# Optimization experiments

Measured on AMD Instinct MI355X. Metric: run time of the kernel, lower is better.

## Reference

```python
import jax, jax.numpy as jnp
import numpy as np

BETA = 0.25  # commitment_beta


def setup_inputs() -> dict:
    key = jax.random.key(0)
    k1, k2 = jax.random.split(key)
    x = jax.random.normal(k1, (16, 256, 32, 32), dtype=jnp.float32)
    # codebook weight: (n_embed + 1, embed_dim); last row is the padding idx (zeros)
    weight = jax.random.normal(k2, (8193, 256), dtype=jnp.float32) * 0.05
    weight = weight.at[-1].set(0.0)
    return {"x": x, "weight": weight}


def reference(x, weight):
    # Eval-mode forward of VectorQuantize2 (accept_image_fmap=True, no EMA update).
    B, C, H, W = x.shape
    xf = jnp.transpose(x, (0, 2, 3, 1)).reshape(B, H * W, C)  # b (h w) c
    emb = weight[:-1]  # [N, C], drop padding row
    # squared euclidean distance; argmin identical to torch.cdist argmin
    d2 = (
        jnp.sum(xf * xf, axis=-1, keepdims=True)
        - 2.0 * jnp.einsum("bnc,kc->bnk", xf, emb)
        + jnp.sum(emb * emb, axis=-1)
    )  # [B, HW, N]
    code = jnp.argmin(d2, axis=-1)  # [B, HW]
    x_q = emb[code]  # [B, HW, C]
    loss = BETA * jnp.mean((jax.lax.stop_gradient(x_q) - xf) ** 2) + jnp.mean(
        (x_q - jax.lax.stop_gradient(xf)) ** 2
    )
    # straight-through estimator
    xq_st = xf + jax.lax.stop_gradient(x_q - xf)
    xq_out = jnp.transpose(xq_st.reshape(B, H, W, C), (0, 3, 1, 2))  # b c h w
    code_out = code.reshape(B, H, W)
    return xq_out, loss, code_out
```

## Files before the change

kernel.cpp:

```cpp
#include <hip/hip_runtime.h>
#include <hip/hip_bf16.h>


#define N_ROWS   16384
#define KCODES   8192
#define DIM      256
#define LOSS_OFF 4194304
#define CODE_OFF 4194305
#define MARGIN_ACC 0.006f

typedef _Float16 half8  __attribute__((ext_vector_type(8)));
typedef _Float16 half4v __attribute__((ext_vector_type(4)));
typedef float    float4v __attribute__((ext_vector_type(4)));
typedef unsigned long long u64;

__device__ __forceinline__ unsigned umax32(unsigned a, unsigned b) { return a > b ? a : b; }
__device__ __forceinline__ unsigned umin32(unsigned a, unsigned b) { return a < b ? a : b; }
__device__ __forceinline__ void gll16(const _Float16* g, _Float16* l) {
  __builtin_amdgcn_global_load_lds((const __attribute__((address_space(1))) void*)g,
                                   (__attribute__((address_space(3))) void*)l, 16, 0, 0);
}


__global__ __launch_bounds__(256) void k_prep(const float* __restrict__ x, _Float16* __restrict__ xh,
                                              const float* __restrict__ wt, _Float16* __restrict__ eh,
                                              float* __restrict__ en2c, double* __restrict__ dacc) {
  __shared__ float lsx[128 * 65];
  __shared__ __align__(16) _Float16 ls[8192];
  __shared__ float es[32];
  int t = threadIdx.x;
  int lane = t & 63, wv = t >> 6;
  if (blockIdx.x < 128) {
    int blk  = blockIdx.x;
    int row0 = blk * 128;
    int b    = row0 >> 10;
    int n0   = row0 & 1023;
    const float* xb = x + (size_t)b * 262144 + n0;
    int n_l = t & 127, cg = t >> 7;
    float sxx = 0.f;
    for (int cc = 0; cc < 4; ++cc) {
      if (cc) __syncthreads();
      for (int j = 0; j < 32; ++j) {
        int c = cc * 64 + cg * 32 + j;
        float v = xb[(size_t)c * 1024 + n_l];
        sxx = fmaf(v, v, sxx);
        lsx[n_l * 65 + (c & 63)] = v;
      }
      __syncthreads();
#pragma unroll
      for (int i = 0; i < 4; ++i) {
        int unit = i * 256 + t;
        int rl = unit >> 3, p = unit & 7;
        const float* src = &lsx[rl * 65 + p * 8];
        half8 h;
#pragma unroll
        for (int k2 = 0; k2 < 8; ++k2) h[k2] = (_Float16)src[k2];
        int p7 = p ^ (rl & 7);
        *(half8*)&xh[(size_t)blk * 32768 + (size_t)cc * 8192 + (size_t)rl * 64 + p7 * 8] = h;
      }
    }
#pragma unroll
    for (int d = 32; d; d >>= 1) sxx += __shfl_xor(sxx, d);
    __syncthreads();
    if (lane == 0) lsx[wv] = sxx;
    __syncthreads();
    if (t == 0) atomicAdd(&dacc[0], (double)(lsx[0] + lsx[1] + lsx[2] + lsx[3]));
  } else {
    int blk  = blockIdx.x - 128;
    int k0 = blk * 32;
    const float* wb = wt + (size_t)k0 * 256;
    for (int i = 0; i < 8; ++i) {
      int lin = i * 1024 + t * 4;
      float4v v = *(const float4v*)&wb[lin];
      half4v h; float ss = 0.f;
#pragma unroll
      for (int j = 0; j < 4; ++j) { h[j] = (_Float16)v[j]; ss = fmaf(v[j], v[j], ss); }
      *(half4v*)&ls[lin] = h;
#pragma unroll
      for (int d = 32; d; d >>= 1) ss += __shfl_xor(ss, d);
      if (lane == 0) es[i * 4 + wv] = ss;
    }
    __syncthreads();
    size_t tb = (size_t)(k0 >> 7) * 32768;
    for (int i = 0; i < 4; ++i) {
      int u = i * 256 + t;
      int code_l = u >> 5;
      int cu = u & 31, chunk = cu >> 3, p = cu & 7;
      int kgl = k0 + code_l;
      int kg = p ^ (kgl & 7);
      half8 h = *(half8*)&ls[code_l * 256 + chunk * 64 + kg * 8];
      *(half8*)&eh[tb + (size_t)chunk * 8192 + (size_t)(kgl & 127) * 64 + p * 8] = h;
    }
    if (t < 32) en2c[k0 + t] = 32.0f - 0.5f * es[t];
  }
}

__global__ __launch_bounds__(256) void k_gemm(const _Float16* __restrict__ xh, const _Float16* __restrict__ eh,
                                              const float* __restrict__ en2c,
                                              u64* __restrict__ top2) {
  __shared__ __align__(16) _Float16 As[8192];
  __shared__ __align__(16) _Float16 Bs[8192];
  int t    = threadIdx.x;
  int bx   = blockIdx.x;
  int by   = blockIdx.y;
  int lane = t & 63, w = t >> 6;
  int wr = w & 1, wc = w >> 1;
  int ln15 = lane & 15, q = lane >> 4;
  int q4 = q * 4;

  const _Float16* Ag = eh + (size_t)bx * 32768;
  const _Float16* Bg = xh + (size_t)by * 32768;

  int kwave = bx * 128 + wr * 64;
  float4v cin[4];
#pragma unroll
  for (int mi = 0; mi < 4; ++mi) cin[mi] = *(const float4v*)&en2c[kwave + mi * 16 + q4];

  float4v acc[4][4];
#pragma unroll
  for (int mi = 0; mi < 4; ++mi)
#pragma unroll
    for (int ni = 0; ni < 4; ++ni) acc[mi][ni] = cin[mi];

  int so = (w * 64 + lane) * 8;
  int lo = w * 512;

  for (int ch = 0; ch < 4; ++ch) {
    if (ch) __syncthreads();
    const _Float16* ac = Ag + ch * 8192;
    const _Float16* bc = Bg + ch * 8192;
#pragma unroll
    for (int i = 0; i < 4; ++i) {
      gll16(ac + i * 2048 + so, As + i * 2048 + lo);
      gll16(bc + i * 2048 + so, Bs + i * 2048 + lo);
    }
    __syncthreads();
#pragma unroll
    for (int ks = 0; ks < 2; ++ks) {
      half8 af[4], bf[4];
#pragma unroll
      for (int mi = 0; mi < 4; ++mi) {
        int row = wr * 64 + mi * 16 + ln15;
        af[mi] = *(const half8*)&As[(row * 8 + ((ks * 4 + q) ^ (row & 7))) * 8];
      }
#pragma unroll
      for (int ni = 0; ni < 4; ++ni) {
        int row = wc * 64 + ni * 16 + ln15;
        bf[ni] = *(const half8*)&Bs[(row * 8 + ((ks * 4 + q) ^ (row & 7))) * 8];
      }
#pragma unroll
      for (int mi = 0; mi < 4; ++mi)
#pragma unroll
        for (int ni = 0; ni < 4; ++ni)
          acc[mi][ni] = __builtin_amdgcn_mfma_f32_16x16x32_f16(af[mi], bf[ni], acc[mi][ni], 0, 0, 0);
    }
  }

  __syncthreads();
  u64* ep = (u64*)(void*)As;
  int ibase = wr * 64 + q4;

#pragma unroll
  for (int ni = 0; ni < 4; ++ni) {
    unsigned hi[8], lo2[8];
#pragma unroll
    for (int j = 0; j < 8; ++j) {
      int mi = j >> 1, rb = (j & 1) * 2;
      unsigned p0 = (__float_as_uint(acc[mi][ni][rb])     & 0xFFFFFF80u) | (unsigned)(ibase + mi * 16 + rb);
      unsigned p1 = (__float_as_uint(acc[mi][ni][rb + 1]) & 0xFFFFFF80u) | (unsigned)(ibase + mi * 16 + rb + 1);
      hi[j] = umax32(p0, p1); lo2[j] = umin32(p0, p1);
    }
#pragma unroll
    for (int st = 4; st; st >>= 1)
#pragma unroll
      for (int j = 0; j < 8; ++j) if (j < st) {
        unsigned nb = umax32(hi[j], hi[j + st]);
        unsigned ns = umax32(umin32(hi[j], hi[j + st]), umax32(lo2[j], lo2[j + st]));
        hi[j] = nb; lo2[j] = ns;
      }
    unsigned b = hi[0], s = lo2[0];
#pragma unroll
    for (int d = 16; d < 64; d <<= 1) {
      unsigned ob = __shfl_xor(b, d);
      unsigned os = __shfl_xor(s, d);
      unsigned ns = umax32(umin32(b, ob), umax32(s, os));
      b = umax32(b, ob); s = ns;
    }
    if (q == 0) {
      int rl = wc * 64 + ni * 16 + ln15;
      ep[rl * 2 + wr] = ((u64)b << 32) | s;
    }
  }
  __syncthreads();
  if (t < 128) {
    u64 A = ep[t * 2 + 0], B = ep[t * 2 + 1];
    unsigned a0 = (unsigned)(A >> 32), a1 = (unsigned)A;
    unsigned b0 = (unsigned)(B >> 32), b1 = (unsigned)B;
    unsigned best = umax32(a0, b0);
    unsigned sec  = umax32(umin32(a0, b0), umax32(a1, b1));
    top2[(size_t)bx * 16384 + (size_t)by * 128 + t] = ((u64)best << 32) | sec;
  }
}

__global__ __launch_bounds__(512) void k_out(const u64* __restrict__ top2,
                                             const float* __restrict__ x, const float* __restrict__ w,
                                             float* __restrict__ out,
                                             double* __restrict__ dacc, unsigned* __restrict__ cnt) {
  __shared__ float ect[256 * 65];
  __shared__ double dpart[8];
  int t    = threadIdx.x;
  int lane = t & 63, wv = t >> 6;
  int blk  = blockIdx.x;
  int row0 = blk * 64;
  int b = row0 >> 10, n0 = row0 & 1023;

  double dsum = 0.0;
  for (int j = 0; j < 8; ++j) {
    int rl  = wv * 8 + j;
    int row = row0 + rl;
    u64 e = top2[(size_t)lane * 16384 + row];
    unsigned hi = (unsigned)(e >> 32), lo = (unsigned)e;
    unsigned mx = hi;
#pragma unroll
    for (int d = 1; d < 64; d <<= 1) mx = umax32(mx, __shfl_xor(mx, d));
    float fm = __uint_as_float(mx & 0xFFFFFF80u);
    float th = fm - MARGIN_ACC;
    bool c0 = __uint_as_float(hi & 0xFFFFFF80u) >= th;
    bool c1 = __uint_as_float(lo & 0xFFFFFF80u) >= th;
    u64 bal0 = __ballot(c0), bal1 = __ballot(c1);
    int kbest;
    double d2c;
    if (__popcll(bal0) + __popcll(bal1) <= 1) {
      int l0 = __ffsll((unsigned long long)__ballot(hi == mx)) - 1;
      kbest = l0 * 128 + (int)(__shfl(hi, l0) & 127u);
      d2c = 64.0 - 2.0 * (double)fm;
    } else {
      const float* xr = x + (size_t)b * 262144 + (row & 1023);
      float4v ex;
#pragma unroll
      for (int i = 0; i < 4; ++i) ex[i] = xr[(size_t)(lane * 4 + i) * 1024];
      double bs = 1e300; int bk = 0x7fffffff;
      for (int pass = 0; pass < 2; ++pass) {
        u64 bal = pass ? bal1 : bal0;
        unsigned src = pass ? lo : hi;
        while (bal) {
          int l = __ffsll((unsigned long long)bal) - 1;
          bal &= bal - 1;
          int kc = l * 128 + (int)(__shfl(src, l) & 127u);
          float4v wv4 = *(const float4v*)&w[(size_t)kc * DIM + lane * 4];
          double s = 0.0;
#pragma unroll
          for (int i = 0; i < 4; ++i) { double ev = (double)wv4[i]; s += ev * (ev - 2.0 * (double)ex[i]); }
#pragma unroll
          for (int d = 1; d < 64; d <<= 1) s += __shfl_xor(s, d);
          if (s < bs || (s == bs && kc < bk)) { bs = s; bk = kc; }
        }
      }
      kbest = bk;
      d2c = bs;
    }
    if (lane == 0) { out[CODE_OFF + row] = (float)kbest; dsum += d2c; }
    const float* wrow = w + (size_t)kbest * 256;
#pragma unroll
    for (int i = 0; i < 4; ++i) ect[(i * 64 + lane) * 65 + rl] = wrow[i * 64 + lane];
  }
  __syncthreads();

  const size_t base = (size_t)b * 262144 + n0 + lane;
  for (int j = 0; j < 32; ++j) {
    int c = wv * 32 + j;
    out[base + (size_t)c * 1024] = ect[c * 65 + lane];
  }
  if (lane == 0) dpart[wv] = dsum;
  __syncthreads();
  if (t == 0) {
    double s = dpart[0] + dpart[1] + dpart[2] + dpart[3] + dpart[4] + dpart[5] + dpart[6] + dpart[7];
    atomicAdd(&dacc[1], s);
    __threadfence();
    unsigned old = atomicAdd(cnt, 1u);
    if (old == 255u) {
      __threadfence();
      double sxx = *(volatile double*)&dacc[0];
      double sd2 = *(volatile double*)&dacc[1];
      out[LOSS_OFF] = (float)(1.25 * (sxx + sd2) / 4194304.0);
    }
  }
}

extern "C" void kernel_launch(void* const* d_in, const int* in_sizes, int n_in,
                              void* d_out, int out_size, void* d_ws, size_t ws_size,
                              hipStream_t stream) {
  const float* x = (const float*)d_in[0];
  const float* w = (const float*)d_in[1];
  float* out = (float*)d_out;
  char* ws = (char*)d_ws;
  _Float16* xh   = (_Float16*)(ws);
  _Float16* eh   = (_Float16*)(ws + 8388608);
  float*    en2c = (float*)(ws + 12582912);
  u64*      top2 = (u64*)(ws + 12615680);
  double*   dacc = (double*)(ws + 21004288);
  unsigned* cnt  = (unsigned*)(ws + 21004304);

  hipMemsetAsync(dacc, 0, 24, stream);
  k_prep<<<384, 256, 0, stream>>>(x, xh, w, eh, en2c, dacc);
  k_gemm<<<dim3(64, 128), 256, 0, stream>>>(xh, eh, en2c, top2);
  k_out<<<256, 512, 0, stream>>>(top2, x, w, out, dacc, cnt);
}
```

Measured before the change: 180.0 us.

## Load codebook fragments directly from global into registers, dropping A LDS tile

The codebook half-precision copy is now stored row-major without the swizzled tiled layout, so the prep kernel skips its LDS staging and reshuffle. The GEMM kernel no longer stages the codebook tile in shared memory. Each wave reads its A fragments straight from global memory into registers, and the launch bounds ask for 3 blocks per CU. This halves LDS use per block to raise occupancy and removes the A-side LDS traffic, at the cost of uncoalesced 16-byte global loads that wait on global memory latency instead of the LDS path. The epilogue scratch now reuses the B buffer, which is 16 KB, where it previously used As.

```diff
diff --git a/kernel.cpp b/kernel.cpp
--- a/kernel.cpp
+++ b/kernel.cpp
@@ -26,7 +26,6 @@
                                               const float* __restrict__ wt, _Float16* __restrict__ eh,
                                               float* __restrict__ en2c, double* __restrict__ dacc) {
   __shared__ float lsx[128 * 65];
-  __shared__ __align__(16) _Float16 ls[8192];
   __shared__ float es[32];
   int t = threadIdx.x;
   int lane = t & 63, wv = t >> 6;
@@ -69,36 +68,26 @@
     int blk  = blockIdx.x - 128;
     int k0 = blk * 32;
     const float* wb = wt + (size_t)k0 * 256;
+    _Float16* eb = eh + (size_t)k0 * 256;
     for (int i = 0; i < 8; ++i) {
       int lin = i * 1024 + t * 4;
       float4v v = *(const float4v*)&wb[lin];
       half4v h; float ss = 0.f;
 #pragma unroll
       for (int j = 0; j < 4; ++j) { h[j] = (_Float16)v[j]; ss = fmaf(v[j], v[j], ss); }
-      *(half4v*)&ls[lin] = h;
+      *(half4v*)&eb[lin] = h;
 #pragma unroll
       for (int d = 32; d; d >>= 1) ss += __shfl_xor(ss, d);
       if (lane == 0) es[i * 4 + wv] = ss;
     }
     __syncthreads();
-    size_t tb = (size_t)(k0 >> 7) * 32768;
-    for (int i = 0; i < 4; ++i) {
-      int u = i * 256 + t;
-      int code_l = u >> 5;
-      int cu = u & 31, chunk = cu >> 3, p = cu & 7;
-      int kgl = k0 + code_l;
-      int kg = p ^ (kgl & 7);
-      half8 h = *(half8*)&ls[code_l * 256 + chunk * 64 + kg * 8];
-      *(half8*)&eh[tb + (size_t)chunk * 8192 + (size_t)(kgl & 127) * 64 + p * 8] = h;
-    }
     if (t < 32) en2c[k0 + t] = 32.0f - 0.5f * es[t];
   }
 }
 
-__global__ __launch_bounds__(256) void k_gemm(const _Float16* __restrict__ xh, const _Float16* __restrict__ eh,
-                                              const float* __restrict__ en2c,
-                                              u64* __restrict__ top2) {
-  __shared__ __align__(16) _Float16 As[8192];
+__global__ __launch_bounds__(256, 3) void k_gemm(const _Float16* __restrict__ xh, const _Float16* __restrict__ eh,
+                                                 const float* __restrict__ en2c,
+                                                 u64* __restrict__ top2) {
   __shared__ __align__(16) _Float16 Bs[8192];
   int t    = threadIdx.x;
   int bx   = blockIdx.x;
@@ -108,8 +97,8 @@
   int ln15 = lane & 15, q = lane >> 4;
   int q4 = q * 4;
 
-  const _Float16* Ag = eh + (size_t)bx * 32768;
   const _Float16* Bg = xh + (size_t)by * 32768;
+  const _Float16* Ab = eh + ((size_t)(bx * 128 + wr * 64) + ln15) * 256 + q * 8;
 
   int kwave = bx * 128 + wr * 64;
   float4v cin[4];
@@ -127,22 +116,20 @@
 
   for (int ch = 0; ch < 4; ++ch) {
     if (ch) __syncthreads();
-    const _Float16* ac = Ag + ch * 8192;
     const _Float16* bc = Bg + ch * 8192;
 #pragma unroll
-    for (int i = 0; i < 4; ++i) {
-      gll16(ac + i * 2048 + so, As + i * 2048 + lo);
+    for (int i = 0; i < 4; ++i)
       gll16(bc + i * 2048 + so, Bs + i * 2048 + lo);
-    }
+    half8 af[2][4];
+#pragma unroll
+    for (int ks = 0; ks < 2; ++ks)
+#pragma unroll
+      for (int mi = 0; mi < 4; ++mi)
+        af[ks][mi] = *(const half8*)(Ab + (size_t)mi * 16 * 256 + ch * 64 + ks * 32);
     __syncthreads();
 #pragma unroll
     for (int ks = 0; ks < 2; ++ks) {
-      half8 af[4], bf[4];
-#pragma unroll
-      for (int mi = 0; mi < 4; ++mi) {
-        int row = wr * 64 + mi * 16 + ln15;
-        af[mi] = *(const half8*)&As[(row * 8 + ((ks * 4 + q) ^ (row & 7))) * 8];
-      }
+      half8 bf[4];
 #pragma unroll
       for (int ni = 0; ni < 4; ++ni) {
         int row = wc * 64 + ni * 16 + ln15;
@@ -152,12 +139,12 @@
       for (int mi = 0; mi < 4; ++mi)
 #pragma unroll
         for (int ni = 0; ni < 4; ++ni)
-          acc[mi][ni] = __builtin_amdgcn_mfma_f32_16x16x32_f16(af[mi], bf[ni], acc[mi][ni], 0, 0, 0);
-    }
-  }
-
-  __syncthreads();
-  u64* ep = (u64*)(void*)As;
+          acc[mi][ni] = __builtin_amdgcn_mfma_f32_16x16x32_f16(af[ks][mi], bf[ni], acc[mi][ni], 0, 0, 0);
+    }
+  }
+
+  __syncthreads();
+  u64* ep = (u64*)(void*)Bs;
   int ibase = wr * 64 + q4;
 
 #pragma unroll
```

Measured after the change: 240.6 us. 33.7% more time.

## Split prep blocks per channel chunk, drop memset, widen output kernel to 1024 threads

Applied to the files above, without the earlier changes.

The x-conversion part of k_prep is split so each block handles one 64-channel chunk, giving 512 blocks instead of 128 to raise parallelism. Per-block sum-of-squares partials are written to a buffer and reduced by the last k_out block, which replaces the double atomics. The separate hipMemsetAsync is dropped, with the accumulators zeroed inside k_prep. k_out now uses 1024-thread blocks with fewer rows per wave. This removes one launch and adds latency hiding, but the in-kernel zeroing of dacc by block 0 is only ordered against k_out because the kernels are launched in sequence.

```diff
diff --git a/kernel.cpp b/kernel.cpp
--- a/kernel.cpp
+++ b/kernel.cpp
@@ -24,49 +24,49 @@
 
 __global__ __launch_bounds__(256) void k_prep(const float* __restrict__ x, _Float16* __restrict__ xh,
                                               const float* __restrict__ wt, _Float16* __restrict__ eh,
-                                              float* __restrict__ en2c, double* __restrict__ dacc) {
+                                              float* __restrict__ en2c, float* __restrict__ sxxp,
+                                              double* __restrict__ dacc, unsigned* __restrict__ cnt) {
   __shared__ float lsx[128 * 65];
   __shared__ __align__(16) _Float16 ls[8192];
   __shared__ float es[32];
   int t = threadIdx.x;
   int lane = t & 63, wv = t >> 6;
-  if (blockIdx.x < 128) {
-    int blk  = blockIdx.x;
+  int bid = blockIdx.x;
+  if (bid < 512) {
+    if (bid == 0 && t == 0) { dacc[0] = 0.0; *cnt = 0u; }
+    int blk = bid >> 2, cc = bid & 3;
     int row0 = blk * 128;
     int b    = row0 >> 10;
     int n0   = row0 & 1023;
     const float* xb = x + (size_t)b * 262144 + n0;
     int n_l = t & 127, cg = t >> 7;
     float sxx = 0.f;
-    for (int cc = 0; cc < 4; ++cc) {
-      if (cc) __syncthreads();
-      for (int j = 0; j < 32; ++j) {
-        int c = cc * 64 + cg * 32 + j;
-        float v = xb[(size_t)c * 1024 + n_l];
-        sxx = fmaf(v, v, sxx);
-        lsx[n_l * 65 + (c & 63)] = v;
-      }
-      __syncthreads();
-#pragma unroll
-      for (int i = 0; i < 4; ++i) {
-        int unit = i * 256 + t;
-        int rl = unit >> 3, p = unit & 7;
-        const float* src = &lsx[rl * 65 + p * 8];
-        half8 h;
-#pragma unroll
-        for (int k2 = 0; k2 < 8; ++k2) h[k2] = (_Float16)src[k2];
-        int p7 = p ^ (rl & 7);
-        *(half8*)&xh[(size_t)blk * 32768 + (size_t)cc * 8192 + (size_t)rl * 64 + p7 * 8] = h;
-      }
+    for (int j = 0; j < 32; ++j) {
+      int c = cc * 64 + cg * 32 + j;
+      float v = xb[(size_t)c * 1024 + n_l];
+      sxx = fmaf(v, v, sxx);
+      lsx[n_l * 65 + (c & 63)] = v;
+    }
+    __syncthreads();
+#pragma unroll
+    for (int i = 0; i < 4; ++i) {
+      int unit = i * 256 + t;
+      int rl = unit >> 3, p = unit & 7;
+      const float* src = &lsx[rl * 65 + p * 8];
+      half8 h;
+#pragma unroll
+      for (int k2 = 0; k2 < 8; ++k2) h[k2] = (_Float16)src[k2];
+      int p7 = p ^ (rl & 7);
+      *(half8*)&xh[(size_t)blk * 32768 + (size_t)cc * 8192 + (size_t)rl * 64 + p7 * 8] = h;
     }
 #pragma unroll
     for (int d = 32; d; d >>= 1) sxx += __shfl_xor(sxx, d);
     __syncthreads();
     if (lane == 0) lsx[wv] = sxx;
     __syncthreads();
-    if (t == 0) atomicAdd(&dacc[0], (double)(lsx[0] + lsx[1] + lsx[2] + lsx[3]));
+    if (t == 0) sxxp[bid] = lsx[0] + lsx[1] + lsx[2] + lsx[3];
   } else {
-    int blk  = blockIdx.x - 128;
+    int blk  = bid - 512;
     int k0 = blk * 32;
     const float* wb = wt + (size_t)k0 * 256;
     for (int i = 0; i < 8; ++i) {
@@ -202,12 +202,13 @@
   }
 }
 
-__global__ __launch_bounds__(512) void k_out(const u64* __restrict__ top2,
-                                             const float* __restrict__ x, const float* __restrict__ w,
-                                             float* __restrict__ out,
-                                             double* __restrict__ dacc, unsigned* __restrict__ cnt) {
+__global__ __launch_bounds__(1024) void k_out(const u64* __restrict__ top2,
+                                              const float* __restrict__ x, const float* __restrict__ w,
+                                              float* __restrict__ out, const float* __restrict__ sxxp,
+                                              double* __restrict__ dacc, unsigned* __restrict__ cnt) {
   __shared__ float ect[256 * 65];
-  __shared__ double dpart[8];
+  __shared__ double dpart[16];
+  __shared__ unsigned oldc;
   int t    = threadIdx.x;
   int lane = t & 63, wv = t >> 6;
   int blk  = blockIdx.x;
@@ -215,8 +216,8 @@
   int b = row0 >> 10, n0 = row0 & 1023;
 
   double dsum = 0.0;
-  for (int j = 0; j < 8; ++j) {
-    int rl  = wv * 8 + j;
+  for (int j = 0; j < 4; ++j) {
+    int rl  = wv * 4 + j;
     int row = row0 + rl;
     u64 e = top2[(size_t)lane * 16384 + row];
     unsigned hi = (unsigned)(e >> 32), lo = (unsigned)e;
@@ -267,22 +268,31 @@
   __syncthreads();
 
   const size_t base = (size_t)b * 262144 + n0 + lane;
-  for (int j = 0; j < 32; ++j) {
-    int c = wv * 32 + j;
+  for (int j = 0; j < 16; ++j) {
+    int c = wv * 16 + j;
     out[base + (size_t)c * 1024] = ect[c * 65 + lane];
   }
   if (lane == 0) dpart[wv] = dsum;
   __syncthreads();
   if (t == 0) {
-    double s = dpart[0] + dpart[1] + dpart[2] + dpart[3] + dpart[4] + dpart[5] + dpart[6] + dpart[7];
-    atomicAdd(&dacc[1], s);
+    double s = 0.0;
+#pragma unroll
+    for (int i = 0; i < 16; ++i) s += dpart[i];
+    atomicAdd(&dacc[0], s);
     __threadfence();
-    unsigned old = atomicAdd(cnt, 1u);
-    if (old == 255u) {
+    oldc = atomicAdd(cnt, 1u);
+  }
+  __syncthreads();
+  if (oldc == 255u && t < 64) {
+    float ps = 0.f;
+#pragma unroll
+    for (int i = 0; i < 8; ++i) ps += sxxp[t * 8 + i];
+#pragma unroll
+    for (int d = 32; d; d >>= 1) ps += __shfl_xor(ps, d);
+    if (t == 0) {
       __threadfence();
-      double sxx = *(volatile double*)&dacc[0];
-      double sd2 = *(volatile double*)&dacc[1];
-      out[LOSS_OFF] = (float)(1.25 * (sxx + sd2) / 4194304.0);
+      double sd2 = *(volatile double*)&dacc[0];
+      out[LOSS_OFF] = (float)(1.25 * ((double)ps + sd2) / 4194304.0);
     }
   }
 }
@@ -298,11 +308,11 @@
   _Float16* eh   = (_Float16*)(ws + 8388608);
   float*    en2c = (float*)(ws + 12582912);
   u64*      top2 = (u64*)(ws + 12615680);
-  double*   dacc = (double*)(ws + 21004288);
-  unsigned* cnt  = (unsigned*)(ws + 21004304);
-
-  hipMemsetAsync(dacc, 0, 24, stream);
-  k_prep<<<384, 256, 0, stream>>>(x, xh, w, eh, en2c, dacc);
+  float*    sxxp = (float*)(ws + 21004288);
+  double*   dacc = (double*)(ws + 21006336);
+  unsigned* cnt  = (unsigned*)(ws + 21006344);
+
+  k_prep<<<768, 256, 0, stream>>>(x, xh, w, eh, en2c, sxxp, dacc, cnt);
   k_gemm<<<dim3(64, 128), 256, 0, stream>>>(xh, eh, en2c, top2);
-  k_out<<<256, 512, 0, stream>>>(top2, x, w, out, dacc, cnt);
-}
+  k_out<<<256, 1024, 0, stream>>>(top2, x, w, out, sxxp, dacc, cnt);
+}
```

Result: faster. 171.3 us (-4.8%).
